# Kernel tuning notes

Measured on AMD Instinct MI355X. Metric: run time of the kernel, lower is better.

## Reference

```python
import jax, jax.numpy as jnp
import numpy as np

N_NODES = 100000
N_REL = 500
N_EDGES = 600000
DIM = 128


def setup_inputs() -> dict:
    key = jax.random.key(0)
    ks = jax.random.split(key, 10)
    ent = jax.random.normal(ks[0], (N_NODES, DIM), dtype=jnp.float32)
    rel = jax.random.normal(ks[1], (N_REL, DIM), dtype=jnp.float32)
    edge_index = jax.random.randint(ks[2], (2, N_EDGES), 0, N_NODES, dtype=jnp.int64)
    edge_type = jax.random.randint(ks[3], (N_EDGES,), 0, N_REL, dtype=jnp.int64)
    s = 1.0 / np.sqrt(DIM)
    W_self = jax.random.uniform(ks[4], (DIM, DIM), jnp.float32, -s, s)
    b_self = jax.random.uniform(ks[5], (DIM,), jnp.float32, -s, s)
    W_nei = jax.random.uniform(ks[6], (DIM, DIM), jnp.float32, -s, s)
    b_nei = jax.random.uniform(ks[7], (DIM,), jnp.float32, -s, s)
    W_rel = jax.random.uniform(ks[8], (DIM, DIM), jnp.float32, -s, s)
    b_rel = jax.random.uniform(ks[9], (DIM,), jnp.float32, -s, s)
    return {
        "ent": ent, "rel": rel, "edge_index": edge_index, "edge_type": edge_type,
        "W_self": W_self, "b_self": b_self,
        "W_nei": W_nei, "b_nei": b_nei,
        "W_rel": W_rel, "b_rel": b_rel,
    }


def reference(ent, rel, edge_index, edge_type, W_self, b_self, W_nei, b_nei, W_rel, b_rel):
    src, dst = edge_index[0], edge_index[1]
    # gather -> sigmoid-gate -> scatter-add
    msg = ent[src] * jax.nn.sigmoid(rel[edge_type])          # [E, dim]
    agg = jax.ops.segment_sum(msg, dst, num_segments=ent.shape[0])  # [N, dim]
    out_ent = jax.nn.relu(ent @ W_self.T + b_self + agg @ W_nei.T + b_nei)
    out_rel = rel @ W_rel.T + b_rel
    return (out_ent, out_rel)
```

## Files before the change

### kernel.cpp

```cpp
#include <hip/hip_runtime.h>
#include <hip/hip_bf16.h>
#include <math.h>

#define DIM 128

typedef __bf16 bf8 __attribute__((ext_vector_type(8)));
typedef float f4 __attribute__((ext_vector_type(4)));
typedef float f2 __attribute__((ext_vector_type(2)));

struct __align__(8) bf16x4 { __hip_bfloat162 a, b; };

__global__ __launch_bounds__(256) void prep_kernel(
    const float* __restrict__ rel,
    const float* __restrict__ Ws,
    const float* __restrict__ Wn,
    const float* __restrict__ Wr,
    __hip_bfloat16* __restrict__ sigb,
    __hip_bfloat16* __restrict__ Wcat,
    float* __restrict__ Wt_rel,
    int* __restrict__ offs,
    uint2* __restrict__ spack2,
    int nSig, int nSigTot, int sigBlocks, int N, int R,
    int zeroBlocks, int fillQuads) {
    int b = blockIdx.x;
    if (b < sigBlocks) {
        int i = b * 256 + threadIdx.x;
        if (i < nSigTot) {
            float v = 0.f;
            if (i < nSig) {
                float x = rel[i];
                v = 1.0f / (1.0f + expf(-x));
            }
            sigb[i] = __float2bfloat16(v);
        }
    } else if (b < sigBlocks + 32) {
        int idx = (b - sigBlocks) * 256 + threadIdx.x;
        int j  = idx >> 6;
        int k0 = (idx & 63) * 4;
        const float* src = (k0 < DIM) ? &Ws[j * DIM + k0] : &Wn[j * DIM + (k0 - DIM)];
        float4 v = *(const float4*)src;
        bf16x4 o;
        o.a.x = __float2bfloat16(v.x);
        o.a.y = __float2bfloat16(v.y);
        o.b.x = __float2bfloat16(v.z);
        o.b.y = __float2bfloat16(v.w);
        *(bf16x4*)&Wcat[(size_t)j * 256 + k0] = o;
    } else if (b < sigBlocks + 32 + 64) {
        int id = (b - sigBlocks - 32) * 256 + threadIdx.x;
        int k = id >> 7;
        int j = id & 127;
        Wt_rel[id] = Wr[j * DIM + k];
    } else if (b < sigBlocks + 32 + 64 + zeroBlocks) {
        int i = (b - sigBlocks - 32 - 64) * 256 + threadIdx.x;
        if (i <= N) offs[i] = 0;
    } else {
        int i = (b - sigBlocks - 32 - 64 - zeroBlocks) * 256 + threadIdx.x;
        if (i < fillQuads) {
            unsigned gz = (unsigned)R * 256u;
            uint4 s; s.x = 0u; s.y = gz; s.z = 0u; s.w = gz;
            ((uint4*)spack2)[i] = s;
        }
    }
}

__global__ __launch_bounds__(256) void conv_hist_kernel(
    const float* __restrict__ ent,
    __hip_bfloat16* __restrict__ xcat,
    const int* __restrict__ edge_index,
    int* __restrict__ counts,
    int* __restrict__ rank,
    int N, int E, int convBlocks) {
    if ((int)blockIdx.x < convBlocks) {
        long long tid = (long long)blockIdx.x * 256 + threadIdx.x;
        int row = (int)(tid >> 5);
        int q   = (int)(tid & 31);
        if (row >= N) return;
        float4 v = *(const float4*)&ent[(size_t)row * DIM + q * 4];
        bf16x4 o;
        o.a.x = __float2bfloat16(v.x);
        o.a.y = __float2bfloat16(v.y);
        o.b.x = __float2bfloat16(v.z);
        o.b.y = __float2bfloat16(v.w);
        *(bf16x4*)&xcat[(size_t)row * 256 + q * 4] = o;
    } else {
        int e = (blockIdx.x - convBlocks) * 256 + threadIdx.x;
        if (e < E) {
            rank[e] = atomicAdd(&counts[edge_index[E + e]], 1);
        }
    }
}

#define SCAN_TPB 256
#define SCAN_IPT 4
#define SCAN_IPB 1024

__global__ void scan_pass1(int* __restrict__ data,
                           int* __restrict__ blockSums, int N) {
    __shared__ int ts[SCAN_TPB];
    int t = threadIdx.x;
    int base = blockIdx.x * SCAN_IPB + t * SCAN_IPT;
    int v[SCAN_IPT];
    int s = 0;
    #pragma unroll
    for (int i = 0; i < SCAN_IPT; ++i) {
        int idx = base + i;
        int c = (idx < N) ? data[idx] : 0;
        v[i] = (c + 3) & ~3;
        s += v[i];
    }
    ts[t] = s;
    __syncthreads();
    for (int off = 1; off < SCAN_TPB; off <<= 1) {
        int x = (t >= off) ? ts[t - off] : 0;
        __syncthreads();
        ts[t] += x;
        __syncthreads();
    }
    int excl = ts[t] - s;
    #pragma unroll
    for (int i = 0; i < SCAN_IPT; ++i) {
        int idx = base + i;
        if (idx < N) data[idx] = excl;
        excl += v[i];
    }
    if (t == SCAN_TPB - 1) blockSums[blockIdx.x] = ts[t];
}

__global__ __launch_bounds__(256) void scan_finish_kernel(
    int* __restrict__ offs, const int* __restrict__ blockSums,
    int nb, int N) {
    __shared__ int ps[128];
    __shared__ int eps[128];
    int t = threadIdx.x;
    int v = 0;
    if (t < 128) {
        v = (t < nb) ? blockSums[t] : 0;
        ps[t] = v;
    }
    __syncthreads();
    for (int off = 1; off < 128; off <<= 1) {
        int x = (t >= off && t < 128) ? ps[t - off] : 0;
        __syncthreads();
        if (t < 128) ps[t] += x;
        __syncthreads();
    }
    if (t < 128) eps[t] = ps[t] - v;
    __syncthreads();
    int i = blockIdx.x * 256 + t;
    if (i < N)  offs[i] += eps[i >> 10];
    if (i == N) offs[N] = ps[127];
}

__global__ void scatter_ids_kernel(const int* __restrict__ edge_index,
                                   const int* __restrict__ edge_type,
                                   const int* __restrict__ offs,
                                   const int* __restrict__ rank,
                                   uint2* __restrict__ spack2, int E) {
    int e = blockIdx.x * blockDim.x + threadIdx.x;
    if (e >= E) return;
    int dst = edge_index[E + e];
    int p = offs[dst] + rank[e];
    uint2 w;
    w.x = (unsigned)edge_index[e] << 9;
    w.y = (unsigned)edge_type[e] << 8;
    spack2[p] = w;
}

__global__ __launch_bounds__(256) void agg_relout_kernel(
    const __hip_bfloat16* __restrict__ xcat,
    const __hip_bfloat16* __restrict__ sigb,
    const int* __restrict__ offs,
    const uint2* __restrict__ spack2,
    __hip_bfloat16* __restrict__ xcat_w,
    const float* __restrict__ rel,
    const float* __restrict__ Wt_rel,
    const float* __restrict__ b_rel,
    float* __restrict__ out_rel,
    int N, int R, int aggBlocks) {
    if ((int)blockIdx.x < aggBlocks) {
        int wid  = (int)((blockIdx.x * (long long)256 + threadIdx.x) >> 6);
        int lane = threadIdx.x & 63;
        if (wid >= N) return;
        int beg = __builtin_amdgcn_readfirstlane(offs[wid]);
        int end = __builtin_amdgcn_readfirstlane(offs[wid + 1]);
        const char* xb = (const char*)xcat;
        const char* gb = (const char*)sigb;
        unsigned so = (unsigned)lane * 4;
        f2 accA = (f2){0.f, 0.f};
        f2 accB = (f2){0.f, 0.f};
        for (int e = beg; e < end; e += 4) {
            uint4 q01 = *(const uint4*)(spack2 + e);
            uint4 q23 = *(const uint4*)(spack2 + e + 2);
            __hip_bfloat162 v0 = *(const __hip_bfloat162*)(xb + (q01.x + so));
            __hip_bfloat162 g0 = *(const __hip_bfloat162*)(gb + (q01.y + so));
            __hip_bfloat162 v1 = *(const __hip_bfloat162*)(xb + (q01.z + so));
            __hip_bfloat162 g1 = *(const __hip_bfloat162*)(gb + (q01.w + so));
            __hip_bfloat162 v2 = *(const __hip_bfloat162*)(xb + (q23.x + so));
            __hip_bfloat162 g2 = *(const __hip_bfloat162*)(gb + (q23.y + so));
            __hip_bfloat162 v3 = *(const __hip_bfloat162*)(xb + (q23.z + so));
            __hip_bfloat162 g3 = *(const __hip_bfloat162*)(gb + (q23.w + so));
            f2 vf0 = (f2){__bfloat162float(v0.x), __bfloat162float(v0.y)};
            f2 gf0 = (f2){__bfloat162float(g0.x), __bfloat162float(g0.y)};
            f2 vf1 = (f2){__bfloat162float(v1.x), __bfloat162float(v1.y)};
            f2 gf1 = (f2){__bfloat162float(g1.x), __bfloat162float(g1.y)};
            f2 vf2 = (f2){__bfloat162float(v2.x), __bfloat162float(v2.y)};
            f2 gf2 = (f2){__bfloat162float(g2.x), __bfloat162float(g2.y)};
            f2 vf3 = (f2){__bfloat162float(v3.x), __bfloat162float(v3.y)};
            f2 gf3 = (f2){__bfloat162float(g3.x), __bfloat162float(g3.y)};
            accA += vf0 * gf0;
            accB += vf1 * gf1;
            accA += vf2 * gf2;
            accB += vf3 * gf3;
        }
        f2 s = accA + accB;
        __hip_bfloat162 o;
        o.x = __float2bfloat16(s.x);
        o.y = __float2bfloat16(s.y);
        *(__hip_bfloat162*)&xcat_w[(size_t)wid * 256 + 128 + lane * 2] = o;
    } else {
        __shared__ float rr[2][DIM];
        int idx  = blockIdx.x - aggBlocks;
        int half = threadIdx.x >> 7;
        int col  = threadIdx.x & 127;
        int row  = idx * 2 + half;
        if (row < R) rr[half][col] = rel[(size_t)row * DIM + col];
        __syncthreads();
        if (row >= R) return;
        float acc = b_rel[col];
        #pragma unroll 8
        for (int k = 0; k < DIM; ++k) {
            acc += rr[half][k] * Wt_rel[k * DIM + col];
        }
        out_rel[(size_t)row * DIM + col] = acc;
    }
}

__global__ __launch_bounds__(256) void gemm_mfma_kernel(
    const __hip_bfloat16* xcat,
    const __hip_bfloat16* __restrict__ Wcat,
    const float* __restrict__ b_self,
    const float* __restrict__ b_nei,
    float* out, int N) {
    __shared__ __hip_bfloat16 Bs[128][264];

    int t    = threadIdx.x;
    int wave = t >> 6;
    int lane = t & 63;
    int quad = lane >> 4;
    int r16  = lane & 15;

    {
        int r = t >> 1, h = t & 1;
        const float4* src = (const float4*)&Wcat[(size_t)r * 256 + h * 128];
        #pragma unroll
        for (int i = 0; i < 16; ++i) {
            *(float4*)&Bs[r][h * 128 + i * 8] = src[i];
        }
    }
    __syncthreads();

    int row0 = blockIdx.x * 128 + wave * 32;

    bf8 x[2][8];
    #pragma unroll
    for (int mt = 0; mt < 2; ++mt) {
        int m = row0 + mt * 16 + r16;
        if (m > N - 1) m = N - 1;
        const __hip_bfloat16* xp = &xcat[(size_t)m * 256 + quad * 8];
        #pragma unroll
        for (int ks = 0; ks < 8; ++ks) {
            x[mt][ks] = *(const bf8*)(xp + ks * 32);
        }
    }

    f4 acc[2][8];
    #pragma unroll
    for (int mt = 0; mt < 2; ++mt)
        #pragma unroll
        for (int jt = 0; jt < 8; ++jt)
            acc[mt][jt] = (f4){0.f, 0.f, 0.f, 0.f};

    #pragma unroll
    for (int ks = 0; ks < 8; ++ks) {
        #pragma unroll
        for (int jt = 0; jt < 8; ++jt) {
            bf8 w = *(const bf8*)&Bs[jt * 16 + r16][ks * 32 + quad * 8];
            acc[0][jt] = __builtin_amdgcn_mfma_f32_16x16x32_bf16(w, x[0][ks], acc[0][jt], 0, 0, 0);
            acc[1][jt] = __builtin_amdgcn_mfma_f32_16x16x32_bf16(w, x[1][ks], acc[1][jt], 0, 0, 0);
        }
    }

    f4 bias4[8];
    #pragma unroll
    for (int jt = 0; jt < 8; ++jt) {
        const float4 bs = *(const float4*)&b_self[jt * 16 + quad * 4];
        const float4 bn = *(const float4*)&b_nei[jt * 16 + quad * 4];
        bias4[jt] = (f4){bs.x + bn.x, bs.y + bn.y, bs.z + bn.z, bs.w + bn.w};
    }

    #pragma unroll
    for (int mt = 0; mt < 2; ++mt) {
        int m = row0 + mt * 16 + r16;
        if (m < N) {
            #pragma unroll
            for (int jt = 0; jt < 8; ++jt) {
                f4 v = acc[mt][jt] + bias4[jt];
                float4 o;
                o.x = fmaxf(v[0], 0.f);
                o.y = fmaxf(v[1], 0.f);
                o.z = fmaxf(v[2], 0.f);
                o.w = fmaxf(v[3], 0.f);
                *(float4*)&out[(size_t)m * DIM + jt * 16 + quad * 4] = o;
            }
        }
    }
}

extern "C" void kernel_launch(void* const* d_in, const int* in_sizes, int n_in,
                              void* d_out, int out_size, void* d_ws, size_t ws_size,
                              hipStream_t stream) {
    const float* ent        = (const float*)d_in[0];
    const float* rel        = (const float*)d_in[1];
    const int*   edge_index = (const int*)d_in[2];
    const int*   edge_type  = (const int*)d_in[3];
    const float* W_self     = (const float*)d_in[4];
    const float* b_self     = (const float*)d_in[5];
    const float* W_nei      = (const float*)d_in[6];
    const float* b_nei      = (const float*)d_in[7];
    const float* W_rel      = (const float*)d_in[8];
    const float* b_rel      = (const float*)d_in[9];

    const int N = in_sizes[0] / DIM;
    const int R = in_sizes[1] / DIM;
    const int E = in_sizes[3];

    float* out     = (float*)d_out;
    float* out_rel = out + (size_t)N * DIM;
    __hip_bfloat16* xcat = (__hip_bfloat16*)d_out;

    __hip_bfloat16* sigb = (__hip_bfloat16*)d_ws;
    float* Wt_rel  = (float*)(sigb + (size_t)(R + 1) * DIM);
    __hip_bfloat16* Wcat = (__hip_bfloat16*)(Wt_rel + DIM * DIM);
    int*   offs    = (int*)(Wcat + 128 * 256);
    int*   bsums   = offs + (N + 8);
    int*   rank    = bsums + 128;
    uint2* spack2  = (uint2*)(rank + E);

    const int nSig = R * DIM;
    const int nSigTot = (R + 1) * DIM;
    const int sigBlocks = (nSigTot + 255) / 256;
    const int zeroBlocks = (N + 1 + 255) / 256;
    const int fillQuads = (E + 3 * N) / 2 + 8;
    const int fillBlocks = (fillQuads + 255) / 256;
    const int scanBlocks = (N + SCAN_IPB - 1) / SCAN_IPB;

    prep_kernel<<<sigBlocks + 32 + 64 + zeroBlocks + fillBlocks, 256, 0, stream>>>(
        rel, W_self, W_nei, W_rel, sigb, Wcat, Wt_rel, offs, spack2,
        nSig, nSigTot, sigBlocks, N, R, zeroBlocks, fillQuads);

    {
        int convBlocks = (int)(((long long)N * 32 + 255) / 256);
        int histBlocks = (E + 255) / 256;
        conv_hist_kernel<<<convBlocks + histBlocks, 256, 0, stream>>>(
            ent, xcat, edge_index, offs, rank, N, E, convBlocks);
    }

    scan_pass1<<<scanBlocks, SCAN_TPB, 0, stream>>>(offs, bsums, N);
    scan_finish_kernel<<<(N + 1 + 255) / 256, 256, 0, stream>>>(
        offs, bsums, scanBlocks, N);

    scatter_ids_kernel<<<(E + 255) / 256, 256, 0, stream>>>(
        edge_index, edge_type, offs, rank, spack2, E);

    {
        int aggBlocks = (int)(((long long)N * 64 + 255) / 256);
        int relBlocks = (R + 1) / 2;
        agg_relout_kernel<<<aggBlocks + relBlocks, 256, 0, stream>>>(
            xcat, sigb, offs, spack2, xcat, rel, Wt_rel, b_rel, out_rel,
            N, R, aggBlocks);
    }

    {
        int blocks = (N + 127) / 128;
        gemm_mfma_kernel<<<blocks, 256, 0, stream>>>(xcat, Wcat, b_self, b_nei, out, N);
    }
}
```

Measured before the change: 221.3 us.

## Process two nodes per wave with 8-byte gathers and grid-stride persistent waves

The aggregation kernel now splits each 64-lane wave into two halves, each handling one destination node with 32 lanes loading 4 bf16 values (8 bytes) per edge instead of 2. The launch switches from one wave per node to a fixed 2048-block grid that walks node pairs with a grid-stride loop. The aim is wider memory transactions per gather, fewer waves and less launch/tail overhead. The two halves of a wave can now have different edge counts, so lanes diverge on the longer node, and the begin/end offsets are no longer wave-uniform scalars.

```diff
diff --git a/kernel.cpp b/kernel.cpp
--- a/kernel.cpp
+++ b/kernel.cpp
@@ -6,7 +6,6 @@
 
 typedef __bf16 bf8 __attribute__((ext_vector_type(8)));
 typedef float f4 __attribute__((ext_vector_type(4)));
-typedef float f2 __attribute__((ext_vector_type(2)));
 
 struct __align__(8) bf16x4 { __hip_bfloat162 a, b; };
 
@@ -178,45 +177,45 @@
     float* __restrict__ out_rel,
     int N, int R, int aggBlocks) {
     if ((int)blockIdx.x < aggBlocks) {
-        int wid  = (int)((blockIdx.x * (long long)256 + threadIdx.x) >> 6);
-        int lane = threadIdx.x & 63;
-        if (wid >= N) return;
-        int beg = __builtin_amdgcn_readfirstlane(offs[wid]);
-        int end = __builtin_amdgcn_readfirstlane(offs[wid + 1]);
+        int wid   = blockIdx.x * 4 + (threadIdx.x >> 6);
+        int lane  = threadIdx.x & 63;
+        int h     = lane >> 5;
+        int s     = lane & 31;
+        unsigned so = (unsigned)s * 8;
         const char* xb = (const char*)xcat;
         const char* gb = (const char*)sigb;
-        unsigned so = (unsigned)lane * 4;
-        f2 accA = (f2){0.f, 0.f};
-        f2 accB = (f2){0.f, 0.f};
-        for (int e = beg; e < end; e += 4) {
-            uint4 q01 = *(const uint4*)(spack2 + e);
-            uint4 q23 = *(const uint4*)(spack2 + e + 2);
-            __hip_bfloat162 v0 = *(const __hip_bfloat162*)(xb + (q01.x + so));
-            __hip_bfloat162 g0 = *(const __hip_bfloat162*)(gb + (q01.y + so));
-            __hip_bfloat162 v1 = *(const __hip_bfloat162*)(xb + (q01.z + so));
-            __hip_bfloat162 g1 = *(const __hip_bfloat162*)(gb + (q01.w + so));
-            __hip_bfloat162 v2 = *(const __hip_bfloat162*)(xb + (q23.x + so));
-            __hip_bfloat162 g2 = *(const __hip_bfloat162*)(gb + (q23.y + so));
-            __hip_bfloat162 v3 = *(const __hip_bfloat162*)(xb + (q23.z + so));
-            __hip_bfloat162 g3 = *(const __hip_bfloat162*)(gb + (q23.w + so));
-            f2 vf0 = (f2){__bfloat162float(v0.x), __bfloat162float(v0.y)};
-            f2 gf0 = (f2){__bfloat162float(g0.x), __bfloat162float(g0.y)};
-            f2 vf1 = (f2){__bfloat162float(v1.x), __bfloat162float(v1.y)};
-            f2 gf1 = (f2){__bfloat162float(g1.x), __bfloat162float(g1.y)};
-            f2 vf2 = (f2){__bfloat162float(v2.x), __bfloat162float(v2.y)};
-            f2 gf2 = (f2){__bfloat162float(g2.x), __bfloat162float(g2.y)};
-            f2 vf3 = (f2){__bfloat162float(v3.x), __bfloat162float(v3.y)};
-            f2 gf3 = (f2){__bfloat162float(g3.x), __bfloat162float(g3.y)};
-            accA += vf0 * gf0;
-            accB += vf1 * gf1;
-            accA += vf2 * gf2;
-            accB += vf3 * gf3;
-        }
-        f2 s = accA + accB;
-        __hip_bfloat162 o;
-        o.x = __float2bfloat16(s.x);
-        o.y = __float2bfloat16(s.y);
-        *(__hip_bfloat162*)&xcat_w[(size_t)wid * 256 + 128 + lane * 2] = o;
+        int nPairs = (N + 1) >> 1;
+        int nWaves = aggBlocks * 4;
+        for (int p = wid; p < nPairs; p += nWaves) {
+            int node = p * 2 + h;
+            int beg = 0, end = 0;
+            if (node < N) { beg = offs[node]; end = offs[node + 1]; }
+            float a0 = 0.f, a1 = 0.f, a2 = 0.f, a3 = 0.f;
+            for (int e = beg; e < end; e += 4) {
+                uint4 q01 = *(const uint4*)(spack2 + e);
+                uint4 q23 = *(const uint4*)(spack2 + e + 2);
+                #define SLOT(px, py) { \
+                    bf16x4 v = *(const bf16x4*)(xb + (px + so)); \
+                    bf16x4 g = *(const bf16x4*)(gb + (py + so)); \
+                    a0 += __bfloat162float(v.a.x) * __bfloat162float(g.a.x); \
+                    a1 += __bfloat162float(v.a.y) * __bfloat162float(g.a.y); \
+                    a2 += __bfloat162float(v.b.x) * __bfloat162float(g.b.x); \
+                    a3 += __bfloat162float(v.b.y) * __bfloat162float(g.b.y); }
+                SLOT(q01.x, q01.y);
+                SLOT(q01.z, q01.w);
+                SLOT(q23.x, q23.y);
+                SLOT(q23.z, q23.w);
+                #undef SLOT
+            }
+            if (node < N) {
+                bf16x4 o;
+                o.a.x = __float2bfloat16(a0);
+                o.a.y = __float2bfloat16(a1);
+                o.b.x = __float2bfloat16(a2);
+                o.b.y = __float2bfloat16(a3);
+                *(bf16x4*)&xcat_w[(size_t)node * 256 + 128 + s * 4] = o;
+            }
+        }
     } else {
         __shared__ float rr[2][DIM];
         int idx  = blockIdx.x - aggBlocks;
@@ -373,7 +372,7 @@
         edge_index, edge_type, offs, rank, spack2, E);
 
     {
-        int aggBlocks = (int)(((long long)N * 64 + 255) / 256);
+        int aggBlocks = 2048;
         int relBlocks = (R + 1) / 2;
         agg_relout_kernel<<<aggBlocks + relBlocks, 256, 0, stream>>>(
             xcat, sigb, offs, spack2, xcat, rel, Wt_rel, b_rel, out_rel,
```

Measured after the change: 230.2 us. +4.0%, slower.
